# Kernel tuning notes

Measured on AMD Instinct MI355X. Metric: run time of the kernel, lower is better.

## Reference

```python
import jax, jax.numpy as jnp
import numpy as np

N, C0, C1 = 8192, 64, 32
P0 = C0 * (C0 + 1) // 2        # 2080 symmetric 0e x 0e pairs
P1 = C1 * (C1 + 1) // 2        # 528 symmetric 1o x 1o pairs -> 0e and 2e
A1 = C1 * (C1 - 1) // 2        # 496 antisymmetric 1o x 1o pairs -> 1e
M0 = C0 + P0 + P1              # 2672 invariant (0e) multiplicities after concat
M1 = C1 + C0 * C1              # 2080 1o multiplicities after concat
NUM_IRREPS = M0 + M1 + A1 + P1 # 5776 total irrep channels (gates)
OUT0, OUT1, OUT1E, OUT2 = 64, 32, 16, 16


def _basis2e():
    # 5 orthonormal (Frobenius) symmetric traceless 3x3 basis matrices: l=2 projection
    s2 = 1.0 / np.sqrt(2.0); s6 = 1.0 / np.sqrt(6.0)
    B = np.zeros((5, 3, 3), np.float32)
    B[0, 0, 1] = B[0, 1, 0] = s2          # xy
    B[1, 1, 2] = B[1, 2, 1] = s2          # yz
    B[2, 0, 2] = B[2, 2, 0] = s2          # xz
    B[3, 0, 0] = s2; B[3, 1, 1] = -s2     # x^2 - y^2
    B[4, 0, 0] = B[4, 1, 1] = -s6; B[4, 2, 2] = 2 * s6  # 2z^2 - x^2 - y^2
    return B


def setup_inputs() -> dict:
    key = jax.random.key(0)
    ks = jax.random.split(key, 8)
    def w(k, shape, fan_in):
        return jax.random.normal(k, shape, jnp.float32) / np.sqrt(fan_in)
    return {
        'x_s': jax.random.normal(ks[0], (N, C0), jnp.float32),
        'x_v': jax.random.normal(ks[1], (N, C1, 3), jnp.float32),
        'mlp_w1': w(ks[2], (M0, M0), M0),
        'mlp_w2': w(ks[3], (M0, NUM_IRREPS), M0),
        'w0': w(ks[4], (M0, OUT0), M0),
        'w1o': w(ks[5], (M1, OUT1), M1),
        'w1e': w(ks[6], (A1, OUT1E), A1),
        'w2e': w(ks[7], (P1, OUT2), P1),
    }


def _forward(x_s, x_v, mlp_w1, mlp_w2, w0, w1o, w1e, w2e):
    n = x_s.shape[0]
    iu0a, iu0b = np.triu_indices(C0)
    c0 = np.where(iu0a == iu0b, 1.0 / np.sqrt(2.0), 1.0).astype(np.float32)
    iu1a, iu1b = np.triu_indices(C1)
    c1 = np.where(iu1a == iu1b, 1.0 / np.sqrt(2.0), 1.0).astype(np.float32)
    ila, ilb = np.triu_indices(C1, k=1)
    B = jnp.asarray(_basis2e())
    # --- tensor square (Clebsch-Gordan contractions) ---
    # 0e x 0e -> 0e (symmetric pairs)
    ss = x_s[:, iu0a] * x_s[:, iu0b] * c0                                   # [n, P0]
    # 1o x 1o symmetric pairs -> 0e (dot) and 2e (sym traceless)
    va, vb = x_v[:, iu1a], x_v[:, iu1b]                                      # [n, P1, 3]
    vv0 = jnp.sum(va * vb, axis=-1) * (c1 / np.sqrt(3.0))                    # [n, P1]
    vv2 = jnp.einsum('npi,npj,kij->npk', va, vb, B) * c1[None, :, None]      # [n, P1, 5]
    # 1o x 1o antisymmetric pairs -> 1e (cross product)
    vv1e = jnp.cross(x_v[:, ila], x_v[:, ilb]) / np.sqrt(2.0)                # [n, A1, 3]
    # 0e x 1o -> 1o
    sv = (x_s[:, :, None, None] * x_v[:, None, :, :]).reshape(n, C0 * C1, 3) # [n, C0*C1, 3]
    # --- concatenate with original features, grouped by irrep ---
    f0 = jnp.concatenate([x_s, ss, vv0], axis=-1)   # [n, M0] invariants
    f1 = jnp.concatenate([x_v, sv], axis=1)         # [n, M1, 3]
    # --- gating MLP on invariants -> one gate per irrep channel ---
    g = jax.nn.silu(f0 @ mlp_w1) @ mlp_w2           # [n, NUM_IRREPS]
    g0 = g[:, :M0]
    g1 = g[:, M0:M0 + M1]
    g1e = g[:, M0 + M1:M0 + M1 + A1]
    g2 = g[:, M0 + M1 + A1:]
    f0 = f0 * g0
    f1 = f1 * g1[:, :, None]
    f1e = vv1e * g1e[:, :, None]
    f2 = vv2 * g2[:, :, None]
    # --- equivariant linear to output irreps (per-l channel mixing) ---
    o0 = f0 @ w0                                    # [n, OUT0]
    o1 = jnp.einsum('nci,co->noi', f1, w1o)         # [n, OUT1, 3]
    o1e = jnp.einsum('nci,co->noi', f1e, w1e)       # [n, OUT1E, 3]
    o2 = jnp.einsum('ncm,co->nom', f2, w2e)         # [n, OUT2, 5]
    return jnp.concatenate([o0, o1.reshape(n, -1), o1e.reshape(n, -1), o2.reshape(n, -1)], axis=-1)


def reference(x_s, x_v, mlp_w1, mlp_w2, w0, w1o, w1e, w2e):
    return _forward(x_s, x_v, mlp_w1, mlp_w2, w0, w1o, w1e, w2e)
```

## Files before the change

### kernel.cpp

```cpp
#include <hip/hip_runtime.h>
#include <hip/hip_bf16.h>
#include <stdint.h>

#define N_ROWS 8192
#define M0C 2672
#define M1C 2080
#define A1C 496
#define P1C 528
#define KP  2688
#define NP2 5888
#define NIR 5776

typedef __attribute__((ext_vector_type(8))) _Float16 half8;
typedef __attribute__((ext_vector_type(4))) float floatx4;

__device__ __forceinline__ void async_copy16(const _Float16* g, _Float16* l) {
  __builtin_amdgcn_global_load_lds(
      (__attribute__((address_space(1))) void*)(g),
      (__attribute__((address_space(3))) void*)(l), 16, 0, 0);
}


__global__ __launch_bounds__(256) void transpose_cvt_kernel(
    const float* __restrict__ src, _Float16* __restrict__ dst,
    int srcR, int srcC, int dstC) {
  __shared__ float tile[32][33];
  const int t = threadIdx.x, tx = t & 31, ty = t >> 5;
  const int bx = blockIdx.x, by = blockIdx.y;
#pragma unroll
  for (int i = 0; i < 4; ++i) {
    int sr = bx * 32 + ty + i * 8;
    int sc = by * 32 + tx;
    tile[ty + i * 8][tx] = (sr < srcR && sc < srcC) ? src[(size_t)sr * srcC + sc] : 0.f;
  }
  __syncthreads();
#pragma unroll
  for (int i = 0; i < 4; ++i) {
    int dr = by * 32 + ty + i * 8;
    int dc = bx * 32 + tx;
    dst[(size_t)dr * dstC + dc] = (_Float16)tile[tx][ty + i * 8];
  }
}

__device__ __forceinline__ void triu_ab(int p, int C, int& a, int& b) {
  float fC = (float)C + 0.5f;
  int ai = (int)(fC - sqrtf(fC * fC - 2.0f * (float)p));
  if (ai < 0) ai = 0;
  while (ai > 0 && ai * C - ai * (ai - 1) / 2 > p) --ai;
  while ((ai + 1) * C - (ai + 1) * ai / 2 <= p) ++ai;
  a = ai;
  b = p - (ai * C - ai * (ai - 1) / 2) + ai;
}

__global__ __launch_bounds__(256) void build_f0_kernel(
    const float* __restrict__ xs_g, const float* __restrict__ xv_g,
    _Float16* __restrict__ f0p) {
  __shared__ float xs[64];
  __shared__ float xv[96];
  const int t = threadIdx.x;
  const size_t n = blockIdx.x;
  if (t < 64) xs[t] = xs_g[n * 64 + t];
  else if (t < 160) xv[t - 64] = xv_g[n * 96 + (t - 64)];
  __syncthreads();
  for (int c = t; c < KP; c += 256) {
    float v;
    if (c < 64) {
      v = xs[c];
    } else if (c < 2144) {
      int a, b;
      triu_ab(c - 64, 64, a, b);
      v = xs[a] * xs[b] * ((a == b) ? 0.70710678118654752f : 1.f);
    } else if (c < M0C) {
      int a, b;
      triu_ab(c - 2144, 32, a, b);
      float d = xv[a * 3] * xv[b * 3] + xv[a * 3 + 1] * xv[b * 3 + 1] +
                xv[a * 3 + 2] * xv[b * 3 + 2];
      v = d * ((a == b) ? 0.70710678118654752f : 1.f) * 0.57735026918962576f;
    } else {
      v = 0.f;
    }
    f0p[n * KP + c] = (_Float16)v;
  }
}

template <bool SILU>
__global__ __launch_bounds__(256, 3) void gemm_kernel(
    const _Float16* __restrict__ A, const _Float16* __restrict__ B,
    _Float16* __restrict__ C, int K, int lda, int ldb, int ldc) {
  __shared__ alignas(16) _Float16 As[128 * 32];
  __shared__ alignas(16) _Float16 Bs[128 * 32];
  const int tid = threadIdx.x;
  const size_t row0 = (size_t)blockIdx.y * 128;
  const size_t col0 = (size_t)blockIdx.x * 128;

  const _Float16* ga[2];
  const _Float16* gb[2];
  _Float16* la[2];
  _Float16* lb[2];
#pragma unroll
  for (int i = 0; i < 2; ++i) {
    int c = tid + i * 256;
    int r = c >> 2;
    int scol = (c & 3) ^ ((r >> 1) & 3);
    ga[i] = A + (row0 + r) * lda + scol * 8;
    gb[i] = B + (col0 + r) * ldb + scol * 8;
    la[i] = &As[c * 8];
    lb[i] = &Bs[c * 8];
  }

  const int lane = tid & 63;
  const int wave = tid >> 6;
  const int wm = (wave & 1) * 64;
  const int wn = (wave >> 1) * 64;
  const int m16 = lane & 15;
  const int quad = lane >> 4;
  const int sw8 = (quad ^ ((m16 >> 1) & 3)) * 8;
  int aoff[4], boff[4];
#pragma unroll
  for (int i = 0; i < 4; ++i) {
    aoff[i] = (wm + i * 16 + m16) * 32 + sw8;
    boff[i] = (wn + i * 16 + m16) * 32 + sw8;
  }

  floatx4 acc[4][4] = {};

  for (int k = 0; k < K; k += 32) {
    if (k) __syncthreads();
#pragma unroll
    for (int i = 0; i < 2; ++i) {
      async_copy16(ga[i] + k, la[i]);
      async_copy16(gb[i] + k, lb[i]);
    }
    __syncthreads();

    half8 af[4], bf[4];
#pragma unroll
    for (int i = 0; i < 4; ++i) af[i] = *(const half8*)&As[aoff[i]];
#pragma unroll
    for (int j = 0; j < 4; ++j) bf[j] = *(const half8*)&Bs[boff[j]];
#pragma unroll
    for (int i = 0; i < 4; ++i)
#pragma unroll
      for (int j = 0; j < 4; ++j)
        acc[i][j] = __builtin_amdgcn_mfma_f32_16x16x32_f16(af[i], bf[j], acc[i][j], 0, 0, 0);
  }

#pragma unroll
  for (int i = 0; i < 4; ++i) {
    size_t r = row0 + wm + i * 16 + quad * 4;
#pragma unroll
    for (int j = 0; j < 4; ++j) {
      size_t cc = col0 + wn + j * 16 + m16;
#pragma unroll
      for (int rr = 0; rr < 4; ++rr) {
        float v = acc[i][j][rr];
        if (SILU) v = v / (1.f + __expf(-v));
        C[(r + rr) * ldc + cc] = (_Float16)v;
      }
    }
  }
}

__global__ __launch_bounds__(256) void epi0_kernel(
    const _Float16* __restrict__ f0p, const _Float16* __restrict__ G,
    const _Float16* __restrict__ w0T, float* __restrict__ out) {
  __shared__ alignas(16) _Float16 As[16 * 32];
  const int t = threadIdx.x;
  const size_t n0 = (size_t)blockIdx.x * 16;
  const int lane = t & 63, wave = t >> 6;
  const int m16 = lane & 15, quad = lane >> 4;
  const int sw8 = (quad ^ ((m16 >> 1) & 3)) * 8;
  const int br = t >> 2;
  const int bsw8 = ((t & 3) ^ ((br >> 1) & 3)) * 8;

  floatx4 acc = {};
  for (int k0 = 0; k0 < KP; k0 += 32) {
    if (k0) __syncthreads();
    if (t < 64) {
      half8 f = *(const half8*)&f0p[(n0 + br) * KP + k0 + bsw8];
      half8 g = *(const half8*)&G[(n0 + br) * NP2 + k0 + bsw8];
      half8 a;
#pragma unroll
      for (int j = 0; j < 8; ++j) a[j] = (_Float16)((float)f[j] * (float)g[j]);
      *(half8*)&As[br * 32 + (t & 3) * 8] = a;
    }
    __syncthreads();
    half8 af = *(const half8*)&As[m16 * 32 + sw8];
    half8 bf = *(const half8*)&w0T[(size_t)(wave * 16 + m16) * KP + k0 + quad * 8];
    acc = __builtin_amdgcn_mfma_f32_16x16x32_f16(af, bf, acc, 0, 0, 0);
  }
#pragma unroll
  for (int rr = 0; rr < 4; ++rr)
    out[(n0 + quad * 4 + rr) * 288 + wave * 16 + m16] = acc[rr];
}

__global__ __launch_bounds__(256) void epi1_kernel(
    const float* __restrict__ xs_g, const float* __restrict__ xv_g,
    const _Float16* __restrict__ G, const _Float16* __restrict__ w1oT,
    float* __restrict__ out) {
  __shared__ float xs[32][64];
  __shared__ float xv[32][96];
  __shared__ alignas(16) _Float16 As[3][32 * 32];
  const int t = threadIdx.x;
  const size_t n0 = (size_t)blockIdx.x * 32;
  for (int idx = t; idx < 32 * 64; idx += 256)
    xs[idx >> 6][idx & 63] = xs_g[(n0 + (idx >> 6)) * 64 + (idx & 63)];
  for (int idx = t; idx < 32 * 96; idx += 256)
    xv[idx / 96][idx % 96] = xv_g[(n0 + idx / 96) * 96 + idx % 96];
  const int lane = t & 63, wave = t >> 6;
  const int m16 = lane & 15, quad = lane >> 4;
  const int sw8 = (quad ^ ((m16 >> 1) & 3)) * 8;
  const int rt = (wave & 1) * 16;
  const int nt = (wave >> 1) * 16;
  const int br = t >> 2;
  const int bchunk = (t & 3) ^ ((br >> 1) & 3);
  const int bc8 = bchunk * 8;

  floatx4 acc[3] = {};
  __syncthreads();
  for (int k0 = 0; k0 < 2080; k0 += 32) {
    if (k0) __syncthreads();
    if (t < 128) {
      half8 g8 = *(const half8*)&G[(n0 + br) * NP2 + M0C + k0 + bc8];
      half8 a0, a1, a2;
      if (k0 == 0) {
#pragma unroll
        for (int j = 0; j < 8; ++j) {
          float g = (float)g8[j];
          int v = bc8 + j;
          a0[j] = (_Float16)(xv[br][v * 3 + 0] * g);
          a1[j] = (_Float16)(xv[br][v * 3 + 1] * g);
          a2[j] = (_Float16)(xv[br][v * 3 + 2] * g);
        }
      } else {
        float xsr = xs[br][(k0 - 32) >> 5];
#pragma unroll
        for (int j = 0; j < 8; ++j) {
          float g = (float)g8[j] * xsr;
          int v = bc8 + j;
          a0[j] = (_Float16)(xv[br][v * 3 + 0] * g);
          a1[j] = (_Float16)(xv[br][v * 3 + 1] * g);
          a2[j] = (_Float16)(xv[br][v * 3 + 2] * g);
        }
      }
      *(half8*)&As[0][br * 32 + (t & 3) * 8] = a0;
      *(half8*)&As[1][br * 32 + (t & 3) * 8] = a1;
      *(half8*)&As[2][br * 32 + (t & 3) * 8] = a2;
    }
    __syncthreads();
    half8 bf = *(const half8*)&w1oT[(size_t)(nt + m16) * 2080 + k0 + quad * 8];
#pragma unroll
    for (int i = 0; i < 3; ++i) {
      half8 af = *(const half8*)&As[i][(rt + m16) * 32 + sw8];
      acc[i] = __builtin_amdgcn_mfma_f32_16x16x32_f16(af, bf, acc[i], 0, 0, 0);
    }
  }
#pragma unroll
  for (int i = 0; i < 3; ++i)
#pragma unroll
    for (int rr = 0; rr < 4; ++rr)
      out[(n0 + rt + quad * 4 + rr) * 288 + 64 + (nt + m16) * 3 + i] = acc[i][rr];
}

__global__ __launch_bounds__(256) void epi1e2_kernel(
    const float* __restrict__ xv_g, const _Float16* __restrict__ G,
    const _Float16* __restrict__ w1eT, const _Float16* __restrict__ w2eT,
    float* __restrict__ out) {
  __shared__ float xv[64][96];
  __shared__ alignas(16) _Float16 As[5][64 * 32];
  __shared__ uint8_t pa[544], pb[544];
  const int t = threadIdx.x;
  const size_t n0 = (size_t)blockIdx.x * 64;
  const int phase = blockIdx.y;
  for (int idx = t; idx < 64 * 96; idx += 256)
    xv[idx / 96][idx % 96] = xv_g[(n0 + idx / 96) * 96 + idx % 96];
  for (int p = t; p < 544; p += 256) {
    int a = 0, b = 0;
    if (phase == 0) {
      if (p < A1C) { triu_ab(p, 31, a, b); b += 1; }
    } else {
      if (p < P1C) triu_ab(p, 32, a, b);
    }
    pa[p] = (uint8_t)a; pb[p] = (uint8_t)b;
  }
  const int lane = t & 63, wave = t >> 6;
  const int m16 = lane & 15, quad = lane >> 4;
  const int sw8 = (quad ^ ((m16 >> 1) & 3)) * 8;
  const int br = t >> 2;
  const int bc8 = ((t & 3) ^ ((br >> 1) & 3)) * 8;
  const int lc8 = (t & 3) * 8;
  const float s2 = 0.70710678118654752f, s6 = 0.40824829046386302f;
  __syncthreads();

  if (phase == 0) {
    floatx4 acc[3] = {};
    for (int k0 = 0; k0 < 512; k0 += 32) {
      if (k0) __syncthreads();
      {
        half8 g8 = *(const half8*)&G[(n0 + br) * NP2 + (M0C + M1C) + k0 + bc8];
        half8 a0, a1, a2;
#pragma unroll
        for (int j = 0; j < 8; ++j) {
          int p = k0 + bc8 + j;
          if (p < A1C) {
            int a = pa[p], b = pb[p];
            float ax = xv[br][a * 3], ay = xv[br][a * 3 + 1], az = xv[br][a * 3 + 2];
            float bx = xv[br][b * 3], by = xv[br][b * 3 + 1], bz = xv[br][b * 3 + 2];
            float g = (float)g8[j] * s2;
            a0[j] = (_Float16)((ay * bz - az * by) * g);
            a1[j] = (_Float16)((az * bx - ax * bz) * g);
            a2[j] = (_Float16)((ax * by - ay * bx) * g);
          } else {
            a0[j] = (_Float16)0.f; a1[j] = (_Float16)0.f; a2[j] = (_Float16)0.f;
          }
        }
        *(half8*)&As[0][br * 32 + lc8] = a0;
        *(half8*)&As[1][br * 32 + lc8] = a1;
        *(half8*)&As[2][br * 32 + lc8] = a2;
      }
      __syncthreads();
      half8 bf = *(const half8*)&w1eT[(size_t)m16 * 512 + k0 + quad * 8];
#pragma unroll
      for (int i = 0; i < 3; ++i) {
        half8 af = *(const half8*)&As[i][(wave * 16 + m16) * 32 + sw8];
        acc[i] = __builtin_amdgcn_mfma_f32_16x16x32_f16(af, bf, acc[i], 0, 0, 0);
      }
    }
#pragma unroll
    for (int i = 0; i < 3; ++i)
#pragma unroll
      for (int rr = 0; rr < 4; ++rr)
        out[(n0 + wave * 16 + quad * 4 + rr) * 288 + 160 + m16 * 3 + i] = acc[i][rr];
  } else {
    floatx4 acc[5] = {};
    for (int k0 = 0; k0 < 544; k0 += 32) {
      if (k0) __syncthreads();
      {
        half8 g8 = *(const half8*)&G[(n0 + br) * NP2 + (M0C + M1C + A1C) + k0 + bc8];
        half8 m0v, m1v, m2v, m3v, m4v;
#pragma unroll
        for (int j = 0; j < 8; ++j) {
          int p = k0 + bc8 + j;
          if (p < P1C) {
            int a = pa[p], b = pb[p];
            float ax = xv[br][a * 3], ay = xv[br][a * 3 + 1], az = xv[br][a * 3 + 2];
            float bx = xv[br][b * 3], by = xv[br][b * 3 + 1], bz = xv[br][b * 3 + 2];
            float c1 = (a == b) ? s2 : 1.f;
            float gw = (float)g8[j] * c1;
            m0v[j] = (_Float16)(s2 * (ax * by + ay * bx) * gw);
            m1v[j] = (_Float16)(s2 * (ay * bz + az * by) * gw);
            m2v[j] = (_Float16)(s2 * (ax * bz + az * bx) * gw);
            m3v[j] = (_Float16)(s2 * (ax * bx - ay * by) * gw);
            m4v[j] = (_Float16)(s6 * (2.f * az * bz - ax * bx - ay * by) * gw);
          } else {
            m0v[j] = (_Float16)0.f; m1v[j] = (_Float16)0.f; m2v[j] = (_Float16)0.f;
            m3v[j] = (_Float16)0.f; m4v[j] = (_Float16)0.f;
          }
        }
        *(half8*)&As[0][br * 32 + lc8] = m0v;
        *(half8*)&As[1][br * 32 + lc8] = m1v;
        *(half8*)&As[2][br * 32 + lc8] = m2v;
        *(half8*)&As[3][br * 32 + lc8] = m3v;
        *(half8*)&As[4][br * 32 + lc8] = m4v;
      }
      __syncthreads();
      half8 bf = *(const half8*)&w2eT[(size_t)m16 * 544 + k0 + quad * 8];
#pragma unroll
      for (int m = 0; m < 5; ++m) {
        half8 af = *(const half8*)&As[m][(wave * 16 + m16) * 32 + sw8];
        acc[m] = __builtin_amdgcn_mfma_f32_16x16x32_f16(af, bf, acc[m], 0, 0, 0);
      }
    }
#pragma unroll
    for (int m = 0; m < 5; ++m)
#pragma unroll
      for (int rr = 0; rr < 4; ++rr)
        out[(n0 + wave * 16 + quad * 4 + rr) * 288 + 208 + m16 * 5 + m] = acc[m][rr];
  }
}

extern "C" void kernel_launch(void* const* d_in, const int* in_sizes, int n_in,
                              void* d_out, int out_size, void* d_ws, size_t ws_size,
                              hipStream_t stream) {
  const float* xs  = (const float*)d_in[0];
  const float* xv  = (const float*)d_in[1];
  const float* w1  = (const float*)d_in[2];
  const float* w2  = (const float*)d_in[3];
  const float* w0  = (const float*)d_in[4];
  const float* w1o = (const float*)d_in[5];
  const float* w1e = (const float*)d_in[6];
  const float* w2e = (const float*)d_in[7];
  float* out = (float*)d_out;

  char* ws = (char*)d_ws;
  size_t off = 0;
  _Float16* w1T = (_Float16*)(ws + off); off += (size_t)KP * KP * 2;
  _Float16* w2T = (_Float16*)(ws + off); off += (size_t)NP2 * KP * 2;
  _Float16* f0p = (_Float16*)(ws + off); off += (size_t)N_ROWS * KP * 2;
  _Float16* H   = (_Float16*)(ws + off); off += (size_t)N_ROWS * KP * 2;
  _Float16* G   = (_Float16*)(ws + off);

  _Float16* w0T  = w1T;
  _Float16* w1oT = (_Float16*)((char*)w1T + 344064);
  _Float16* w1eT = (_Float16*)((char*)w1T + 477184);
  _Float16* w2eT = (_Float16*)((char*)w1T + 509952);

  transpose_cvt_kernel<<<dim3(KP / 32, KP / 32), 256, 0, stream>>>(w1, w1T, M0C, M0C, KP);
  transpose_cvt_kernel<<<dim3(KP / 32, NP2 / 32), 256, 0, stream>>>(w2, w2T, M0C, NIR, KP);
  build_f0_kernel<<<N_ROWS, 256, 0, stream>>>(xs, xv, f0p);
  gemm_kernel<true><<<dim3(KP / 128, N_ROWS / 128), 256, 0, stream>>>(f0p, w1T, H, KP, KP, KP, KP);
  transpose_cvt_kernel<<<dim3(KP / 32, 2), 256, 0, stream>>>(w0, w0T, M0C, 64, KP);
  transpose_cvt_kernel<<<dim3(65, 1), 256, 0, stream>>>(w1o, w1oT, M1C, 32, 2080);
  transpose_cvt_kernel<<<dim3(16, 1), 256, 0, stream>>>(w1e, w1eT, A1C, 16, 512);
  transpose_cvt_kernel<<<dim3(17, 1), 256, 0, stream>>>(w2e, w2eT, P1C, 16, 544);
  gemm_kernel<false><<<dim3(NP2 / 128, N_ROWS / 128), 256, 0, stream>>>(H, w2T, G, KP, KP, KP, NP2);
  epi0_kernel<<<512, 256, 0, stream>>>(f0p, G, w0T, out);
  epi1_kernel<<<256, 256, 0, stream>>>(xs, xv, G, w1oT, out);
  epi1e2_kernel<<<dim3(128, 2), 256, 0, stream>>>(xv, G, w1eT, w2eT, out);
}
```

Measured before the change: 899.0 us.

## Swizzle GEMM block order and widen epilogue K-tiles to 64

```diff
diff --git a/kernel.cpp b/kernel.cpp
--- a/kernel.cpp
+++ b/kernel.cpp
@@ -10,6 +10,7 @@
 #define KP  2688
 #define NP2 5888
 #define NIR 5776
+#define M1P 2112
 
 typedef __attribute__((ext_vector_type(8))) _Float16 half8;
 typedef __attribute__((ext_vector_type(4))) float floatx4;
@@ -19,7 +20,6 @@
       (__attribute__((address_space(1))) void*)(g),
       (__attribute__((address_space(3))) void*)(l), 16, 0, 0);
 }
-
 
 __global__ __launch_bounds__(256) void transpose_cvt_kernel(
     const float* __restrict__ src, _Float16* __restrict__ dst,
@@ -90,8 +90,13 @@
   __shared__ alignas(16) _Float16 As[128 * 32];
   __shared__ alignas(16) _Float16 Bs[128 * 32];
   const int tid = threadIdx.x;
-  const size_t row0 = (size_t)blockIdx.y * 128;
-  const size_t col0 = (size_t)blockIdx.x * 128;
+  const int gx = gridDim.x;
+  const int id = blockIdx.y * gx + blockIdx.x;
+  const int jj = id >> 3;
+  const int by = (id & 7) * 8 + (jj & 7);
+  const int bx = jj >> 3;
+  const size_t row0 = (size_t)by * 128;
+  const size_t col0 = (size_t)bx * 128;
 
   const _Float16* ga[2];
   const _Float16* gb[2];
@@ -164,34 +169,44 @@
 __global__ __launch_bounds__(256) void epi0_kernel(
     const _Float16* __restrict__ f0p, const _Float16* __restrict__ G,
     const _Float16* __restrict__ w0T, float* __restrict__ out) {
-  __shared__ alignas(16) _Float16 As[16 * 32];
+  __shared__ alignas(16) _Float16 As[32 * 64];
   const int t = threadIdx.x;
-  const size_t n0 = (size_t)blockIdx.x * 16;
+  const size_t n0 = (size_t)blockIdx.x * 32;
   const int lane = t & 63, wave = t >> 6;
   const int m16 = lane & 15, quad = lane >> 4;
-  const int sw8 = (quad ^ ((m16 >> 1) & 3)) * 8;
-  const int br = t >> 2;
-  const int bsw8 = ((t & 3) ^ ((br >> 1) & 3)) * 8;
-
-  floatx4 acc = {};
-  for (int k0 = 0; k0 < KP; k0 += 32) {
+  const int rt = (wave & 1) * 16;
+  const int ctb = (wave >> 1) * 32;
+  const int br = t >> 3, p = t & 7;
+  const int l8 = (p ^ (br & 7)) * 8;
+
+  floatx4 acc[2] = {};
+  for (int k0 = 0; k0 < KP; k0 += 64) {
     if (k0) __syncthreads();
-    if (t < 64) {
-      half8 f = *(const half8*)&f0p[(n0 + br) * KP + k0 + bsw8];
-      half8 g = *(const half8*)&G[(n0 + br) * NP2 + k0 + bsw8];
+    {
+      half8 f = *(const half8*)&f0p[(n0 + br) * KP + k0 + l8];
+      half8 g = *(const half8*)&G[(n0 + br) * NP2 + k0 + l8];
       half8 a;
 #pragma unroll
       for (int j = 0; j < 8; ++j) a[j] = (_Float16)((float)f[j] * (float)g[j]);
-      *(half8*)&As[br * 32 + (t & 3) * 8] = a;
+      *(half8*)&As[br * 64 + p * 8] = a;
     }
     __syncthreads();
-    half8 af = *(const half8*)&As[m16 * 32 + sw8];
-    half8 bf = *(const half8*)&w0T[(size_t)(wave * 16 + m16) * KP + k0 + quad * 8];
-    acc = __builtin_amdgcn_mfma_f32_16x16x32_f16(af, bf, acc, 0, 0, 0);
-  }
-#pragma unroll
-  for (int rr = 0; rr < 4; ++rr)
-    out[(n0 + quad * 4 + rr) * 288 + wave * 16 + m16] = acc[rr];
+#pragma unroll
+    for (int kk = 0; kk < 2; ++kk) {
+      int q = kk * 4 + quad;
+      half8 af = *(const half8*)&As[(rt + m16) * 64 + (q ^ (m16 & 7)) * 8];
+#pragma unroll
+      for (int c = 0; c < 2; ++c) {
+        half8 bf = *(const half8*)&w0T[(size_t)(ctb + c * 16 + m16) * KP + k0 + kk * 32 + quad * 8];
+        acc[c] = __builtin_amdgcn_mfma_f32_16x16x32_f16(af, bf, acc[c], 0, 0, 0);
+      }
+    }
+  }
+#pragma unroll
+  for (int c = 0; c < 2; ++c)
+#pragma unroll
+    for (int rr = 0; rr < 4; ++rr)
+      out[(n0 + rt + quad * 4 + rr) * 288 + ctb + c * 16 + m16] = acc[c][rr];
 }
 
 __global__ __launch_bounds__(256) void epi1_kernel(
@@ -200,7 +215,7 @@
     float* __restrict__ out) {
   __shared__ float xs[32][64];
   __shared__ float xv[32][96];
-  __shared__ alignas(16) _Float16 As[3][32 * 32];
+  __shared__ alignas(16) _Float16 As[3][32 * 64];
   const int t = threadIdx.x;
   const size_t n0 = (size_t)blockIdx.x * 32;
   for (int idx = t; idx < 32 * 64; idx += 256)
@@ -209,57 +224,63 @@
     xv[idx / 96][idx % 96] = xv_g[(n0 + idx / 96) * 96 + idx % 96];
   const int lane = t & 63, wave = t >> 6;
   const int m16 = lane & 15, quad = lane >> 4;
-  const int sw8 = (quad ^ ((m16 >> 1) & 3)) * 8;
   const int rt = (wave & 1) * 16;
-  const int nt = (wave >> 1) * 16;
-  const int br = t >> 2;
-  const int bchunk = (t & 3) ^ ((br >> 1) & 3);
-  const int bc8 = bchunk * 8;
+  const int ct = (wave >> 1) * 16;
+  const int br = t >> 3, p = t & 7;
+  const int l8 = (p ^ (br & 7)) * 8;
 
   floatx4 acc[3] = {};
   __syncthreads();
-  for (int k0 = 0; k0 < 2080; k0 += 32) {
+  for (int k0 = 0; k0 < M1P; k0 += 64) {
     if (k0) __syncthreads();
-    if (t < 128) {
-      half8 g8 = *(const half8*)&G[(n0 + br) * NP2 + M0C + k0 + bc8];
+    {
+      half8 g8 = *(const half8*)&G[(n0 + br) * NP2 + M0C + k0 + l8];
+      int kbase = k0 + l8;
       half8 a0, a1, a2;
-      if (k0 == 0) {
+      if (kbase < 32) {
 #pragma unroll
         for (int j = 0; j < 8; ++j) {
           float g = (float)g8[j];
-          int v = bc8 + j;
+          int v = kbase + j;
           a0[j] = (_Float16)(xv[br][v * 3 + 0] * g);
           a1[j] = (_Float16)(xv[br][v * 3 + 1] * g);
           a2[j] = (_Float16)(xv[br][v * 3 + 2] * g);
         }
       } else {
-        float xsr = xs[br][(k0 - 32) >> 5];
+        int s = (kbase - 32) >> 5;
+        if (s > 63) s = 63;
+        int v0 = (kbase - 32) & 31;
+        float xsr = xs[br][s];
 #pragma unroll
         for (int j = 0; j < 8; ++j) {
           float g = (float)g8[j] * xsr;
-          int v = bc8 + j;
+          int v = v0 + j;
           a0[j] = (_Float16)(xv[br][v * 3 + 0] * g);
           a1[j] = (_Float16)(xv[br][v * 3 + 1] * g);
           a2[j] = (_Float16)(xv[br][v * 3 + 2] * g);
         }
       }
-      *(half8*)&As[0][br * 32 + (t & 3) * 8] = a0;
-      *(half8*)&As[1][br * 32 + (t & 3) * 8] = a1;
-      *(half8*)&As[2][br * 32 + (t & 3) * 8] = a2;
+      *(half8*)&As[0][br * 64 + p * 8] = a0;
+      *(half8*)&As[1][br * 64 + p * 8] = a1;
+      *(half8*)&As[2][br * 64 + p * 8] = a2;
     }
     __syncthreads();
-    half8 bf = *(const half8*)&w1oT[(size_t)(nt + m16) * 2080 + k0 + quad * 8];
-#pragma unroll
-    for (int i = 0; i < 3; ++i) {
-      half8 af = *(const half8*)&As[i][(rt + m16) * 32 + sw8];
-      acc[i] = __builtin_amdgcn_mfma_f32_16x16x32_f16(af, bf, acc[i], 0, 0, 0);
+#pragma unroll
+    for (int kk = 0; kk < 2; ++kk) {
+      int q = kk * 4 + quad;
+      half8 bf = *(const half8*)&w1oT[(size_t)(ct + m16) * M1P + k0 + kk * 32 + quad * 8];
+#pragma unroll
+      for (int i = 0; i < 3; ++i) {
+        half8 af = *(const half8*)&As[i][(rt + m16) * 64 + (q ^ (m16 & 7)) * 8];
+        acc[i] = __builtin_amdgcn_mfma_f32_16x16x32_f16(af, bf, acc[i], 0, 0, 0);
+      }
     }
   }
 #pragma unroll
   for (int i = 0; i < 3; ++i)
 #pragma unroll
     for (int rr = 0; rr < 4; ++rr)
-      out[(n0 + rt + quad * 4 + rr) * 288 + 64 + (nt + m16) * 3 + i] = acc[i][rr];
+      out[(n0 + rt + quad * 4 + rr) * 288 + 64 + (ct + m16) * 3 + i] = acc[i][rr];
 }
 
 __global__ __launch_bounds__(256) void epi1e2_kernel(
@@ -402,19 +423,19 @@
 
   _Float16* w0T  = w1T;
   _Float16* w1oT = (_Float16*)((char*)w1T + 344064);
-  _Float16* w1eT = (_Float16*)((char*)w1T + 477184);
-  _Float16* w2eT = (_Float16*)((char*)w1T + 509952);
+  _Float16* w1eT = (_Float16*)((char*)w1T + 479232);
+  _Float16* w2eT = (_Float16*)((char*)w1T + 512000);
 
   transpose_cvt_kernel<<<dim3(KP / 32, KP / 32), 256, 0, stream>>>(w1, w1T, M0C, M0C, KP);
   transpose_cvt_kernel<<<dim3(KP / 32, NP2 / 32), 256, 0, stream>>>(w2, w2T, M0C, NIR, KP);
   build_f0_kernel<<<N_ROWS, 256, 0, stream>>>(xs, xv, f0p);
   gemm_kernel<true><<<dim3(KP / 128, N_ROWS / 128), 256, 0, stream>>>(f0p, w1T, H, KP, KP, KP, KP);
   transpose_cvt_kernel<<<dim3(KP / 32, 2), 256, 0, stream>>>(w0, w0T, M0C, 64, KP);
-  transpose_cvt_kernel<<<dim3(65, 1), 256, 0, stream>>>(w1o, w1oT, M1C, 32, 2080);
+  transpose_cvt_kernel<<<dim3(M1P / 32, 1), 256, 0, stream>>>(w1o, w1oT, M1C, 32, M1P);
   transpose_cvt_kernel<<<dim3(16, 1), 256, 0, stream>>>(w1e, w1eT, A1C, 16, 512);
   transpose_cvt_kernel<<<dim3(17, 1), 256, 0, stream>>>(w2e, w2eT, P1C, 16, 544);
   gemm_kernel<false><<<dim3(NP2 / 128, N_ROWS / 128), 256, 0, stream>>>(H, w2T, G, KP, KP, KP, NP2);
-  epi0_kernel<<<512, 256, 0, stream>>>(f0p, G, w0T, out);
+  epi0_kernel<<<256, 256, 0, stream>>>(f0p, G, w0T, out);
   epi1_kernel<<<256, 256, 0, stream>>>(xs, xv, G, w1oT, out);
   epi1e2_kernel<<<dim3(128, 2), 256, 0, stream>>>(xv, G, w1eT, w2eT, out);
 }
```

New measurement: 795.6 us. -11.5%, faster.
